# Kernel tuning notes

Hardware: AMD Instinct MI355X
Metric: run time of the kernel (lower is better)

## Reference

```python
import jax, jax.numpy as jnp
import numpy as np

TEMPERATURE = 8.0  # sqrt(d_k=64)


def setup_inputs() -> dict:
    key = jax.random.key(0)
    kq, kk, kv, km = jax.random.split(key, 4)
    B, S, D = 16, 2048, 64
    q = jax.random.normal(kq, (B, S, D), dtype=jnp.float32)
    k = jax.random.normal(kk, (B, S, D), dtype=jnp.float32)
    v = jax.random.normal(kv, (B, S, D), dtype=jnp.float32)
    mask = jax.random.randint(km, (1, S, S), 0, 2, dtype=jnp.int32)
    return {"q": q, "k": k, "v": v, "mask": mask}


def reference(q, k, v, mask):
    # scores: [B, S, S] = (q / temperature) @ k^T
    attn = jnp.einsum('bsd,btd->bst', q / TEMPERATURE, k)
    attn = jnp.where(mask == 0, jnp.float32(-1e9), attn)
    attn = jax.nn.softmax(attn, axis=-1)
    # dropout is identity in eval-mode math (source stores float, not a module)
    output = jnp.einsum('bst,btd->bsd', attn, v)
    return (output, attn)
```

## Files before the change

### kernel.cpp

```cpp
#include <hip/hip_runtime.h>

constexpr int NB = 16;
constexpr int NS = 2048;
constexpr int ND = 64;
constexpr int MTILE = 16;
constexpr int NW32 = NS / 32;

typedef __attribute__((ext_vector_type(8))) short bh8;
typedef __attribute__((ext_vector_type(4))) float f32x4;
typedef __attribute__((ext_vector_type(4))) unsigned short us4;

constexpr int EB_STRIDE = 2048 + 8;

__device__ __forceinline__ unsigned short f2bf(float x) {
  unsigned u = __float_as_uint(x);
  u += 0x7fffu + ((u >> 16) & 1u);
  return (unsigned short)(u >> 16);
}
__device__ __forceinline__ float bf2f(unsigned u16) {
  return __uint_as_float(u16 << 16);
}

__global__ __launch_bounds__(256)
void prep_kv_kernel(const float* __restrict__ v, const float* __restrict__ k,
                    unsigned short* __restrict__ vt, unsigned short* __restrict__ kbf) {
  __shared__ float tile[64][65];
  const int b   = blockIdx.y;
  const int kc  = blockIdx.x;
  const int tid = threadIdx.x;
  const int r0  = tid >> 4;
  const int c0  = (tid & 15) * 4;
  #pragma unroll
  for (int p = 0; p < 4; ++p) {
    const int krow = p * 16 + r0;
    const long base = ((long)(b * NS) + kc * 64 + krow) * ND + c0;
    float4 vv = *(const float4*)(v + base);
    tile[c0 + 0][krow] = vv.x;
    tile[c0 + 1][krow] = vv.y;
    tile[c0 + 2][krow] = vv.z;
    tile[c0 + 3][krow] = vv.w;
    float4 kk4 = *(const float4*)(k + base);
    us4 ko;
    ko.x = f2bf(kk4.x); ko.y = f2bf(kk4.y); ko.z = f2bf(kk4.z); ko.w = f2bf(kk4.w);
    *(us4*)(kbf + base) = ko;
  }
  __syncthreads();
  #pragma unroll
  for (int p = 0; p < 4; ++p) {
    const int d = p * 16 + r0;
    us4 o;
    o.x = f2bf(tile[d][c0 + 0]);
    o.y = f2bf(tile[d][c0 + 1]);
    o.z = f2bf(tile[d][c0 + 2]);
    o.w = f2bf(tile[d][c0 + 3]);
    *(us4*)(vt + ((long)(b * 64 + d)) * NS + kc * 64 + c0) = o;
  }
}

__global__ __launch_bounds__(256)
void maskpack_kernel(const int* __restrict__ mask, unsigned* __restrict__ mbits) {
  const int row = blockIdx.y;
  const int col = blockIdx.x * 256 + threadIdx.x;
  const unsigned long long bal = __ballot(mask[(long)row * NS + col] != 0);
  const int lane = threadIdx.x & 63;
  if (lane == 0)       mbits[row * NW32 + (col >> 5)] = (unsigned)bal;
  else if (lane == 32) mbits[row * NW32 + (col >> 5)] = (unsigned)(bal >> 32);
}

__global__ __launch_bounds__(512, 4)
void sdpa_fused_kernel(const float* __restrict__ q, const unsigned short* __restrict__ kbf,
                       const unsigned* __restrict__ mbits, const unsigned short* __restrict__ vt,
                       float* __restrict__ outO, float* __restrict__ outA)
{
  extern __shared__ char smem[];
  unsigned short* ebuf = (unsigned short*)smem;
  float* rowsumP = (float*)(ebuf + MTILE * EB_STRIDE);
  float* invl    = rowsumP + 16 * 8;
  float* osum    = invl + 16;

  const int tid  = threadIdx.x;
  const int wave = tid >> 6;
  const int lane = tid & 63;
  const int n16  = lane & 15;
  const int quad = lane >> 4;

  const int bid   = blockIdx.y * gridDim.x + blockIdx.x;
  const int swz   = (bid & 7) * 256 + (bid >> 3);
  const int b     = swz >> 7;
  const int mbase = (swz & 127) * MTILE;

  const int col0 = wave * 256;
  const int r0q  = quad * 4;

  bh8 aq[2];
  {
    const float* qp = q + ((long)(b * NS + mbase + n16)) * ND + quad * 8;
    #pragma unroll
    for (int kk = 0; kk < 2; ++kk) {
      float4 x0 = *(const float4*)(qp + kk * 32);
      float4 x1 = *(const float4*)(qp + kk * 32 + 4);
      bh8 f;
      f[0] = f2bf(x0.x * 0.125f); f[1] = f2bf(x0.y * 0.125f);
      f[2] = f2bf(x0.z * 0.125f); f[3] = f2bf(x0.w * 0.125f);
      f[4] = f2bf(x1.x * 0.125f); f[5] = f2bf(x1.y * 0.125f);
      f[6] = f2bf(x1.z * 0.125f); f[7] = f2bf(x1.w * 0.125f);
      aq[kk] = f;
    }
  }

  const unsigned short* kbp = kbf + (long)(b * NS) * ND + quad * 8;
  float rsum[4] = {0.f, 0.f, 0.f, 0.f};

#define LOADG(kf, mw, g) do {                                                   \
    const int kk0 = col0 + (g) * 32;                                            \
    const unsigned short* kp = kbp + (long)(kk0 + n16) * ND;                    \
    kf[0] = *(const bh8*)(kp);                                                  \
    kf[1] = *(const bh8*)(kp + 32);                                             \
    kf[2] = *(const bh8*)(kp + 16 * ND);                                        \
    kf[3] = *(const bh8*)(kp + 16 * ND + 32);                                   \
    _Pragma("unroll")                                                           \
    for (int r = 0; r < 4; ++r)                                                 \
      mw[r] = mbits[(long)(mbase + r0q + r) * NW32 + (kk0 >> 5)];               \
  } while (0)

#define COMPUTEG(kf, mw, g) do {                                                \
    _Pragma("unroll")                                                           \
    for (int h = 0; h < 2; ++h) {                                               \
      f32x4 acc = {0.f, 0.f, 0.f, 0.f};                                         \
      acc = __builtin_amdgcn_mfma_f32_16x16x32_bf16(aq[0], kf[2*h],   acc,0,0,0);\
      acc = __builtin_amdgcn_mfma_f32_16x16x32_bf16(aq[1], kf[2*h+1], acc,0,0,0);\
      const int key = col0 + (g) * 32 + h * 16 + n16;                           \
      _Pragma("unroll")                                                         \
      for (int r = 0; r < 4; ++r) {                                             \
        const unsigned bit = (mw[r] >> (h * 16 + n16)) & 1u;                    \
        const float e = bit ? __expf(acc[r]) : 0.f;                             \
        rsum[r] += e;                                                           \
        ebuf[(r0q + r) * EB_STRIDE + key] = f2bf(e);                            \
      }                                                                         \
    }                                                                           \
  } while (0)

  {
    bh8 kfA[4], kfB[4], kfC[4], kfD[4];
    unsigned mwA[4], mwB[4], mwC[4], mwD[4];
    LOADG(kfA, mwA, 0); LOADG(kfB, mwB, 1); LOADG(kfC, mwC, 2); LOADG(kfD, mwD, 3);
    COMPUTEG(kfA, mwA, 0); LOADG(kfA, mwA, 4);
    COMPUTEG(kfB, mwB, 1); LOADG(kfB, mwB, 5);
    COMPUTEG(kfC, mwC, 2); LOADG(kfC, mwC, 6);
    COMPUTEG(kfD, mwD, 3); LOADG(kfD, mwD, 7);
    COMPUTEG(kfA, mwA, 4);
    COMPUTEG(kfB, mwB, 5);
    COMPUTEG(kfC, mwC, 6);
    COMPUTEG(kfD, mwD, 7);
  }
#undef LOADG
#undef COMPUTEG

  const int dtile = wave & 3;
  const int khalf = wave >> 2;
  const int kb    = khalf * 1024;
  const unsigned short* vrow = vt + ((long)(b * 64 + dtile * 16 + n16)) * NS + kb + quad * 8;
  bh8 vA[2], vB[2], vC[2];
  vA[0] = *(const bh8*)(vrow);        vA[1] = *(const bh8*)(vrow + 32);
  vB[0] = *(const bh8*)(vrow + 64);   vB[1] = *(const bh8*)(vrow + 96);
  vC[0] = *(const bh8*)(vrow + 128);  vC[1] = *(const bh8*)(vrow + 160);

  #pragma unroll
  for (int r = 0; r < 4; ++r) {
    float s = rsum[r];
    s += __shfl_xor(s, 1);
    s += __shfl_xor(s, 2);
    s += __shfl_xor(s, 4);
    s += __shfl_xor(s, 8);
    if (n16 == 0) rowsumP[(r0q + r) * 8 + wave] = s;
  }
  __syncthreads();
  if (tid < 16) {
    float l = 0.f;
    #pragma unroll
    for (int c = 0; c < 8; ++c) l += rowsumP[tid * 8 + c];
    invl[tid] = 1.f / l;
  }
  __syncthreads();

  const unsigned short* ebp = ebuf + n16 * EB_STRIDE + kb + quad * 8;
  bh8 aA[2], aB[2], aC[2];
  aA[0] = *(const bh8*)(ebp);        aA[1] = *(const bh8*)(ebp + 32);
  aB[0] = *(const bh8*)(ebp + 64);   aB[1] = *(const bh8*)(ebp + 96);
  aC[0] = *(const bh8*)(ebp + 128);  aC[1] = *(const bh8*)(ebp + 160);

  f32x4 oacc = {0.f, 0.f, 0.f, 0.f};

#define PVSTEP(p, aa, vv) do {                                                  \
    oacc = __builtin_amdgcn_mfma_f32_16x16x32_bf16(aa[0], vv[0], oacc, 0,0,0);  \
    oacc = __builtin_amdgcn_mfma_f32_16x16x32_bf16(aa[1], vv[1], oacc, 0,0,0);  \
    if ((p) <= 12) {                                                            \
      vv[0] = *(const bh8*)(vrow + ((p)+3) * 64);                               \
      vv[1] = *(const bh8*)(vrow + ((p)+3) * 64 + 32);                          \
      aa[0] = *(const bh8*)(ebp  + ((p)+3) * 64);                               \
      aa[1] = *(const bh8*)(ebp  + ((p)+3) * 64 + 32);                          \
    }                                                                           \
  } while (0)

  PVSTEP(0,  aA, vA); PVSTEP(1,  aB, vB); PVSTEP(2,  aC, vC);
  PVSTEP(3,  aA, vA); PVSTEP(4,  aB, vB); PVSTEP(5,  aC, vC);
  PVSTEP(6,  aA, vA); PVSTEP(7,  aB, vB); PVSTEP(8,  aC, vC);
  PVSTEP(9,  aA, vA); PVSTEP(10, aB, vB); PVSTEP(11, aC, vC);
  PVSTEP(12, aA, vA); PVSTEP(13, aB, vB); PVSTEP(14, aC, vC);
  PVSTEP(15, aA, vA);
#undef PVSTEP

  if (khalf == 1) *(f32x4*)(osum + (dtile * 64 + lane) * 4) = oacc;

  {
    float* aout = outA + ((long)(b * NS + mbase)) * NS;
    const int c4 = tid * 4;
    f32x4 il4[4];
    il4[0] = *(const f32x4*)(invl);
    il4[1] = *(const f32x4*)(invl + 4);
    il4[2] = *(const f32x4*)(invl + 8);
    il4[3] = *(const f32x4*)(invl + 12);
    #pragma unroll
    for (int p = 0; p < 16; ++p) {
      const float il = il4[p >> 2][p & 3];
      uint2 raw = *(const uint2*)(ebuf + p * EB_STRIDE + c4);
      f32x4 o;
      o[0] = bf2f(raw.x & 0xffffu) * il;
      o[1] = bf2f(raw.x >> 16)     * il;
      o[2] = bf2f(raw.y & 0xffffu) * il;
      o[3] = bf2f(raw.y >> 16)     * il;
      __builtin_nontemporal_store(o, (f32x4*)(aout + (long)p * NS + c4));
    }
  }

  __syncthreads();
  if (khalf == 0) {
    f32x4 other = *(const f32x4*)(osum + (dtile * 64 + lane) * 4);
    #pragma unroll
    for (int r = 0; r < 4; ++r) {
      const int lrow = quad * 4 + r;
      __builtin_nontemporal_store(
          (oacc[r] + other[r]) * invl[lrow],
          outO + ((long)(b * NS + mbase + lrow)) * ND + dtile * 16 + n16);
    }
  }
}

extern "C" void kernel_launch(void* const* d_in, const int* in_sizes, int n_in,
                              void* d_out, int out_size, void* d_ws, size_t ws_size,
                              hipStream_t stream) {
  const float* q    = (const float*)d_in[0];
  const float* k    = (const float*)d_in[1];
  const float* v    = (const float*)d_in[2];
  const int*   mask = (const int*)d_in[3];
  float* outO = (float*)d_out;
  float* outA = outO + (long)NB * NS * ND;

  unsigned short* vt    = (unsigned short*)d_ws;
  unsigned short* kbf   = vt + (long)NB * ND * NS;
  unsigned*       mbits = (unsigned*)(kbf + (long)NB * NS * ND);

  prep_kv_kernel<<<dim3(NS / 64, NB), 256, 0, stream>>>(v, k, vt, kbf);
  maskpack_kernel<<<dim3(NS / 256, NS), 256, 0, stream>>>(mask, mbits);

  const size_t lds = (size_t)(MTILE * EB_STRIDE) * sizeof(short)
                   + (size_t)(16 * 8 + 16 + 4 * 64 * 4) * sizeof(float);
  hipFuncSetAttribute((const void*)sdpa_fused_kernel,
                      hipFuncAttributeMaxDynamicSharedMemorySize, (int)lds);
  sdpa_fused_kernel<<<dim3(NS / MTILE, NB), 512, lds, stream>>>(q, kbf, mbits, vt, outO, outA);
}
```

Baseline: 400.7 us.

## Fuse mask packing into prep kernel, use exp2 with folded log2e, add MFMA priority

Folds the mask bit-packing into the K/V prep kernel so each block packs four mask rows, removing one kernel launch. It also folds log2(e) into the Q scale so the softmax can use exp2f instead of __expf, and wraps the MFMA pairs in s_setprio raises to favour matrix issue. The mask fusion assumes the prep grid (32x16 = 512 blocks times 4 rows) exactly covers the 2048 mask rows, and it adds serial ballot work to each prep block.

```diff
diff --git a/kernel.cpp b/kernel.cpp
--- a/kernel.cpp
+++ b/kernel.cpp
@@ -23,13 +23,33 @@
 
 __global__ __launch_bounds__(256)
 void prep_kv_kernel(const float* __restrict__ v, const float* __restrict__ k,
-                    unsigned short* __restrict__ vt, unsigned short* __restrict__ kbf) {
+                    const int* __restrict__ mask,
+                    unsigned short* __restrict__ vt, unsigned short* __restrict__ kbf,
+                    unsigned* __restrict__ mbits) {
   __shared__ float tile[64][65];
   const int b   = blockIdx.y;
   const int kc  = blockIdx.x;
   const int tid = threadIdx.x;
   const int r0  = tid >> 4;
   const int c0  = (tid & 15) * 4;
+
+  {
+    const int lin  = b * 32 + kc;
+    const int wv   = tid >> 6;
+    const int lane = tid & 63;
+    #pragma unroll
+    for (int rr = 0; rr < 4; ++rr) {
+      const int row = lin * 4 + rr;
+      #pragma unroll
+      for (int i = 0; i < 8; ++i) {
+        const int col = wv * 512 + i * 64 + lane;
+        const unsigned long long bal = __ballot(mask[(long)row * NS + col] != 0);
+        if (lane == 0)       mbits[row * NW32 + (col >> 5)] = (unsigned)bal;
+        else if (lane == 32) mbits[row * NW32 + (col >> 5)] = (unsigned)(bal >> 32);
+      }
+    }
+  }
+
   #pragma unroll
   for (int p = 0; p < 4; ++p) {
     const int krow = p * 16 + r0;
@@ -57,16 +77,6 @@
   }
 }
 
-__global__ __launch_bounds__(256)
-void maskpack_kernel(const int* __restrict__ mask, unsigned* __restrict__ mbits) {
-  const int row = blockIdx.y;
-  const int col = blockIdx.x * 256 + threadIdx.x;
-  const unsigned long long bal = __ballot(mask[(long)row * NS + col] != 0);
-  const int lane = threadIdx.x & 63;
-  if (lane == 0)       mbits[row * NW32 + (col >> 5)] = (unsigned)bal;
-  else if (lane == 32) mbits[row * NW32 + (col >> 5)] = (unsigned)(bal >> 32);
-}
-
 __global__ __launch_bounds__(512, 4)
 void sdpa_fused_kernel(const float* __restrict__ q, const unsigned short* __restrict__ kbf,
                        const unsigned* __restrict__ mbits, const unsigned short* __restrict__ vt,
@@ -92,6 +102,7 @@
   const int col0 = wave * 256;
   const int r0q  = quad * 4;
 
+  constexpr float QSCALE = 0.125f * 1.44269504088896340736f;
   bh8 aq[2];
   {
     const float* qp = q + ((long)(b * NS + mbase + n16)) * ND + quad * 8;
@@ -100,10 +111,10 @@
       float4 x0 = *(const float4*)(qp + kk * 32);
       float4 x1 = *(const float4*)(qp + kk * 32 + 4);
       bh8 f;
-      f[0] = f2bf(x0.x * 0.125f); f[1] = f2bf(x0.y * 0.125f);
-      f[2] = f2bf(x0.z * 0.125f); f[3] = f2bf(x0.w * 0.125f);
-      f[4] = f2bf(x1.x * 0.125f); f[5] = f2bf(x1.y * 0.125f);
-      f[6] = f2bf(x1.z * 0.125f); f[7] = f2bf(x1.w * 0.125f);
+      f[0] = f2bf(x0.x * QSCALE); f[1] = f2bf(x0.y * QSCALE);
+      f[2] = f2bf(x0.z * QSCALE); f[3] = f2bf(x0.w * QSCALE);
+      f[4] = f2bf(x1.x * QSCALE); f[5] = f2bf(x1.y * QSCALE);
+      f[6] = f2bf(x1.z * QSCALE); f[7] = f2bf(x1.w * QSCALE);
       aq[kk] = f;
     }
   }
@@ -127,13 +138,15 @@
     _Pragma("unroll")                                                           \
     for (int h = 0; h < 2; ++h) {                                               \
       f32x4 acc = {0.f, 0.f, 0.f, 0.f};                                         \
+      __builtin_amdgcn_s_setprio(1);                                            \
       acc = __builtin_amdgcn_mfma_f32_16x16x32_bf16(aq[0], kf[2*h],   acc,0,0,0);\
       acc = __builtin_amdgcn_mfma_f32_16x16x32_bf16(aq[1], kf[2*h+1], acc,0,0,0);\
+      __builtin_amdgcn_s_setprio(0);                                            \
       const int key = col0 + (g) * 32 + h * 16 + n16;                           \
       _Pragma("unroll")                                                         \
       for (int r = 0; r < 4; ++r) {                                             \
         const unsigned bit = (mw[r] >> (h * 16 + n16)) & 1u;                    \
-        const float e = bit ? __expf(acc[r]) : 0.f;                             \
+        const float e = bit ? exp2f(acc[r]) : 0.f;                              \
         rsum[r] += e;                                                           \
         ebuf[(r0q + r) * EB_STRIDE + key] = f2bf(e);                            \
       }                                                                         \
@@ -192,8 +205,10 @@
   f32x4 oacc = {0.f, 0.f, 0.f, 0.f};
 
 #define PVSTEP(p, aa, vv) do {                                                  \
+    __builtin_amdgcn_s_setprio(1);                                              \
     oacc = __builtin_amdgcn_mfma_f32_16x16x32_bf16(aa[0], vv[0], oacc, 0,0,0);  \
     oacc = __builtin_amdgcn_mfma_f32_16x16x32_bf16(aa[1], vv[1], oacc, 0,0,0);  \
+    __builtin_amdgcn_s_setprio(0);                                              \
     if ((p) <= 12) {                                                            \
       vv[0] = *(const bh8*)(vrow + ((p)+3) * 64);                               \
       vv[1] = *(const bh8*)(vrow + ((p)+3) * 64 + 32);                          \
@@ -260,8 +275,7 @@
   unsigned short* kbf   = vt + (long)NB * ND * NS;
   unsigned*       mbits = (unsigned*)(kbf + (long)NB * NS * ND);
 
-  prep_kv_kernel<<<dim3(NS / 64, NB), 256, 0, stream>>>(v, k, vt, kbf);
-  maskpack_kernel<<<dim3(NS / 256, NS), 256, 0, stream>>>(mask, mbits);
+  prep_kv_kernel<<<dim3(NS / 64, NB), 256, 0, stream>>>(v, k, mask, vt, kbf, mbits);
 
   const size_t lds = (size_t)(MTILE * EB_STRIDE) * sizeof(short)
                    + (size_t)(16 * 8 + 16 + 4 * 64 * 4) * sizeof(float);
```

Result: slower. 424.5 us (+5.9%).
